# Kernel optimization log

Measured on AMD Instinct MI355X. Metric: run time of the kernel, lower is better.

The kernel has to match this reference:

```python
import jax, jax.numpy as jnp
import numpy as np

TEMP = 0.5  # temperature from init_kwargs
EPS = 1e-8  # torch.nn.CosineSimilarity eps


def setup_inputs() -> dict:
    key = jax.random.key(0)
    k1, k2 = jax.random.split(key)
    B, D = 4096, 128
    return {
        "z_i": jax.random.normal(k1, (B, D), dtype=jnp.float32),
        "z_j": jax.random.normal(k2, (B, D), dtype=jnp.float32),
    }


def reference(z_i, z_j):
    B = z_i.shape[0]          # batch_size * world_size
    N = 2 * B
    z = jnp.concatenate([z_i, z_j], axis=0)              # [N, D]
    zn = z / jnp.maximum(jnp.linalg.norm(z, axis=1, keepdims=True), EPS)
    sim = (zn @ zn.T) / TEMP                             # [N, N] cosine sim / temp
    # positives: sim[i, i+B] and sim[i+B, i]
    pos = jnp.concatenate([jnp.diagonal(sim, offset=B), jnp.diagonal(sim, offset=-B)])  # [N]
    # CE with label 0 over [pos, negatives]; since the positive-pair entry equals pos,
    # denominator = sum_{j != i} exp(sim[i, j])  (only the diagonal is excluded)
    eye = jnp.eye(N, dtype=bool)
    sim_masked = jnp.where(eye, -jnp.inf, sim)
    lse = jax.nn.logsumexp(sim_masked, axis=1)           # [N]
    loss = jnp.sum(lse - pos) / N                        # reduction='sum' then /= N
    return loss
```

## Files before the change

kernel.cpp:

```cpp
#include <hip/hip_runtime.h>
#include <hip/hip_bf16.h>


typedef short bfrag __attribute__((ext_vector_type(8)));
typedef float f32x4 __attribute__((ext_vector_type(4)));

static __device__ __forceinline__ unsigned short f2bf_rne(float x) {
    unsigned u = __float_as_uint(x);
    return (unsigned short)((u + 0x7fffu + ((u >> 16) & 1u)) >> 16);
}
static __device__ __forceinline__ float bf2f(unsigned short b) {
    return __uint_as_float(((unsigned)b) << 16);
}

__global__ __launch_bounds__(256) void nt_norm_pair(
        const float* __restrict__ zi, const float* __restrict__ zj,
        unsigned short* __restrict__ zn, float* __restrict__ diag,
        float* __restrict__ pos, float* __restrict__ sumexp) {
    constexpr int B = 4096, D = 128;
    const int wave = threadIdx.x >> 6, lane = threadIdx.x & 63;
    const int p = blockIdx.x * 4 + wave;
    float2 a = reinterpret_cast<const float2*>(zi + (size_t)p * D)[lane];
    float2 b = reinterpret_cast<const float2*>(zj + (size_t)p * D)[lane];
    float sa = a.x * a.x + a.y * a.y;
    float sb = b.x * b.x + b.y * b.y;
    #pragma unroll
    for (int m = 32; m; m >>= 1) { sa += __shfl_xor(sa, m); sb += __shfl_xor(sb, m); }
    float ia = 1.f / fmaxf(sqrtf(sa), 1e-8f);
    float ib = 1.f / fmaxf(sqrtf(sb), 1e-8f);
    unsigned short a0 = f2bf_rne(a.x * ia), a1 = f2bf_rne(a.y * ia);
    unsigned short b0 = f2bf_rne(b.x * ib), b1 = f2bf_rne(b.y * ib);
    float fa0 = bf2f(a0), fa1 = bf2f(a1), fb0 = bf2f(b0), fb1 = bf2f(b1);
    float da = fa0 * fa0 + fa1 * fa1;
    float db = fb0 * fb0 + fb1 * fb1;
    float cr = fa0 * fb0 + fa1 * fb1;
    #pragma unroll
    for (int m = 32; m; m >>= 1) {
        da += __shfl_xor(da, m); db += __shfl_xor(db, m); cr += __shfl_xor(cr, m);
    }
    reinterpret_cast<unsigned*>(zn + (size_t)p * D)[lane] =
        (unsigned)a0 | ((unsigned)a1 << 16);
    reinterpret_cast<unsigned*>(zn + (size_t)(p + B) * D)[lane] =
        (unsigned)b0 | ((unsigned)b1 << 16);
    if (lane == 0) {
        diag[p] = da; diag[p + B] = db;
        pos[p] = 2.f * cr; pos[p + B] = 2.f * cr;
        sumexp[p] = 0.f; sumexp[p + B] = 0.f;
    }
}

__global__ __launch_bounds__(256, 2) void nt_gram_sym(
        const unsigned short* __restrict__ zn, float* __restrict__ sumexp) {
    const int c = blockIdx.x;
    const int y = blockIdx.y;
    const int T  = (y == 0) ? 1 : ((y == 8 && c >= 32) ? 3 : 4);
    const int d0 = (y == 0) ? 0 : 4 * (y - 1) + 1;

    __shared__ short buf[2][128][128];

    const short* zs = (const short*)zn;
    const int tid = threadIdx.x, wid = tid >> 6, lane = tid & 63;
    const int wj = wid >> 1, wi = wid & 1;
    const int lr = lane & 15, lk = lane >> 4;

    bfrag ca[4][4];
    {
        const int rbase = c * 128 + wj * 64;
        #pragma unroll
        for (int ks = 0; ks < 4; ++ks)
            #pragma unroll
            for (int f = 0; f < 4; ++f)
                ca[ks][f] = *reinterpret_cast<const bfrag*>(
                    zs + (size_t)(rbase + f * 16 + lr) * 128 + ks * 32 + lk * 8);
    }
    asm volatile("s_waitcnt vmcnt(0)" ::: "memory");

    auto STAGE = [&](int t, int slot) {
        const int srow = ((c + d0 + t) & 63) * 128;
        #pragma unroll
        for (int q = 0; q < 8; ++q) {
            const int cbase = (q * 4 + wid) * 64;
            const int chunk = cbase + lane;
            const int r = chunk >> 4;
            const int cpos = chunk & 15;
            const int csrc = cpos ^ (r & 7);
            const short* g = zs + (size_t)(srow + r) * 128 + csrc * 8;
            __builtin_amdgcn_global_load_lds(
                (const __attribute__((address_space(1))) void*)g,
                (__attribute__((address_space(3))) void*)(
                    &buf[slot][0][0] + (size_t)cbase * 8),
                16, 0, 0);
        }
    };

    STAGE(0, 0);

    constexpr float K_E = 2.8853900817779268f;
    float jp[16];
    #pragma unroll
    for (int q = 0; q < 16; ++q) jp[q] = 0.f;

    for (int t = 0; t < T; ++t) {
        const bool more = (t + 1 < T);
        if (more) STAGE(t + 1, (t + 1) & 1);
        if (t == 0) {
            if (more) asm volatile("s_waitcnt vmcnt(8)" ::: "memory");
            else      asm volatile("s_waitcnt vmcnt(0)" ::: "memory");
        } else {
            if (more) asm volatile("s_waitcnt vmcnt(12)" ::: "memory");
            else      asm volatile("s_waitcnt vmcnt(4)" ::: "memory");
        }
        __builtin_amdgcn_s_barrier();

        const int srow = ((c + d0 + t) & 63) * 128;
        f32x4 acc[4][4] = {};
        #pragma unroll
        for (int ks = 0; ks < 4; ++ks) {
            bfrag cb[4];
            #pragma unroll
            for (int f = 0; f < 4; ++f) {
                const int r = wi * 64 + f * 16 + lr;
                const int cc = (ks * 4 + lk) ^ (lr & 7);
                cb[f] = *reinterpret_cast<const bfrag*>(&buf[t & 1][r][cc * 8]);
            }
            #pragma unroll
            for (int fj = 0; fj < 4; ++fj)
                #pragma unroll
                for (int fi = 0; fi < 4; ++fi)
                    acc[fj][fi] = __builtin_amdgcn_mfma_f32_16x16x32_bf16(
                        ca[ks][fj], cb[fi], acc[fj][fi], 0, 0, 0);
        }

        const float cw = (d0 + t) ? 1.f : 0.f;
        #pragma unroll
        for (int fi = 0; fi < 4; ++fi) {
            float s = 0.f;
            #pragma unroll
            for (int fj = 0; fj < 4; ++fj)
                #pragma unroll
                for (int r = 0; r < 4; ++r) {
                    const float e = exp2f(acc[fj][fi][r] * K_E);
                    s += e;
                    jp[fj * 4 + r] += e * cw;
                }
            s += __shfl_xor(s, 16);
            s += __shfl_xor(s, 32);
            if (lk == 0) atomicAdd(&sumexp[srow + wi * 64 + fi * 16 + lr], s);
        }
        __builtin_amdgcn_s_barrier();
    }

    float myv = 0.f;
    #pragma unroll
    for (int tt = 0; tt < 16; ++tt) {
        float v = jp[tt];
        v += __shfl_xor(v, 1);
        v += __shfl_xor(v, 2);
        v += __shfl_xor(v, 4);
        v += __shfl_xor(v, 8);
        if (lr == tt) myv = v;
    }
    atomicAdd(&sumexp[c * 128 + wj * 64 + (lr >> 2) * 16 + lk * 4 + (lr & 3)], myv);
}

__global__ __launch_bounds__(1024) void nt_finalize(
        const float* __restrict__ sumexp, const float* __restrict__ diag,
        const float* __restrict__ pos, float* __restrict__ out) {
    constexpr int N = 8192;
    constexpr float K_E = 2.8853900817779268f;
    float s = 0.f;
    for (int i = threadIdx.x; i < N; i += 1024)
        s += __logf(sumexp[i] - exp2f(diag[i] * K_E)) - pos[i];
    #pragma unroll
    for (int m = 32; m; m >>= 1) s += __shfl_xor(s, m);
    __shared__ float red[16];
    if ((threadIdx.x & 63) == 0) red[threadIdx.x >> 6] = s;
    __syncthreads();
    if (threadIdx.x == 0) {
        float t = 0.f;
        #pragma unroll
        for (int w = 0; w < 16; ++w) t += red[w];
        out[0] = t * (1.0f / (float)N);
    }
}

extern "C" void kernel_launch(void* const* d_in, const int* in_sizes, int n_in,
                              void* d_out, int out_size, void* d_ws, size_t ws_size,
                              hipStream_t stream) {
    const float* zi = (const float*)d_in[0];
    const float* zj = (const float*)d_in[1];
    float* out = (float*)d_out;

    char* ws = (char*)d_ws;
    unsigned short* zn = (unsigned short*)ws;
    float* sumexp = (float*)(ws + 2 * 1024 * 1024);
    float* diag   = (float*)(ws + 2 * 1024 * 1024 + 1 * 32768);
    float* pos    = (float*)(ws + 2 * 1024 * 1024 + 2 * 32768);

    nt_norm_pair<<<1024, 256, 0, stream>>>(zi, zj, zn, diag, pos, sumexp);
    nt_gram_sym<<<dim3(64, 9), 256, 0, stream>>>(zn, sumexp);
    nt_finalize<<<1, 1024, 0, stream>>>(sumexp, diag, pos, out);
}
```

Before: 37.88 us.

## Shrink gram tiles to 64 rows, prescale operand by exp2 constant

```diff
diff --git a/kernel.cpp b/kernel.cpp
--- a/kernel.cpp
+++ b/kernel.cpp
@@ -15,9 +15,11 @@
 
 __global__ __launch_bounds__(256) void nt_norm_pair(
         const float* __restrict__ zi, const float* __restrict__ zj,
-        unsigned short* __restrict__ zn, float* __restrict__ diag,
-        float* __restrict__ pos, float* __restrict__ sumexp) {
+        unsigned short* __restrict__ zn, unsigned short* __restrict__ znK,
+        float* __restrict__ diag, float* __restrict__ pos,
+        float* __restrict__ sumexp) {
     constexpr int B = 4096, D = 128;
+    constexpr float K_E = 2.8853900817779268f;
     const int wave = threadIdx.x >> 6, lane = threadIdx.x & 63;
     const int p = blockIdx.x * 4 + wave;
     float2 a = reinterpret_cast<const float2*>(zi + (size_t)p * D)[lane];
@@ -31,17 +33,23 @@
     unsigned short a0 = f2bf_rne(a.x * ia), a1 = f2bf_rne(a.y * ia);
     unsigned short b0 = f2bf_rne(b.x * ib), b1 = f2bf_rne(b.y * ib);
     float fa0 = bf2f(a0), fa1 = bf2f(a1), fb0 = bf2f(b0), fb1 = bf2f(b1);
-    float da = fa0 * fa0 + fa1 * fa1;
-    float db = fb0 * fb0 + fb1 * fb1;
+    unsigned short aK0 = f2bf_rne(K_E * fa0), aK1 = f2bf_rne(K_E * fa1);
+    unsigned short bK0 = f2bf_rne(K_E * fb0), bK1 = f2bf_rne(K_E * fb1);
+    float da = bf2f(aK0) * fa0 + bf2f(aK1) * fa1;
+    float db = bf2f(bK0) * fb0 + bf2f(bK1) * fb1;
     float cr = fa0 * fb0 + fa1 * fb1;
     #pragma unroll
     for (int m = 32; m; m >>= 1) {
         da += __shfl_xor(da, m); db += __shfl_xor(db, m); cr += __shfl_xor(cr, m);
     }
-    reinterpret_cast<unsigned*>(zn + (size_t)p * D)[lane] =
+    reinterpret_cast<unsigned*>(zn  + (size_t)p * D)[lane] =
         (unsigned)a0 | ((unsigned)a1 << 16);
-    reinterpret_cast<unsigned*>(zn + (size_t)(p + B) * D)[lane] =
+    reinterpret_cast<unsigned*>(zn  + (size_t)(p + B) * D)[lane] =
         (unsigned)b0 | ((unsigned)b1 << 16);
+    reinterpret_cast<unsigned*>(znK + (size_t)p * D)[lane] =
+        (unsigned)aK0 | ((unsigned)aK1 << 16);
+    reinterpret_cast<unsigned*>(znK + (size_t)(p + B) * D)[lane] =
+        (unsigned)bK0 | ((unsigned)bK1 << 16);
     if (lane == 0) {
         diag[p] = da; diag[p + B] = db;
         pos[p] = 2.f * cr; pos[p + B] = 2.f * cr;
@@ -49,37 +57,39 @@
     }
 }
 
-__global__ __launch_bounds__(256, 2) void nt_gram_sym(
-        const unsigned short* __restrict__ zn, float* __restrict__ sumexp) {
+__global__ __launch_bounds__(256, 4) void nt_gram_sym(
+        const unsigned short* __restrict__ zn,
+        const unsigned short* __restrict__ znK,
+        float* __restrict__ sumexp) {
     const int c = blockIdx.x;
     const int y = blockIdx.y;
-    const int T  = (y == 0) ? 1 : ((y == 8 && c >= 32) ? 3 : 4);
+    const int T  = (y == 0) ? 1 : ((y == 16 && c >= 64) ? 3 : 4);
     const int d0 = (y == 0) ? 0 : 4 * (y - 1) + 1;
 
-    __shared__ short buf[2][128][128];
-
-    const short* zs = (const short*)zn;
+    __shared__ short buf[2][64][128];
+
+    const short* zs  = (const short*)zn;
+    const short* zsK = (const short*)znK;
     const int tid = threadIdx.x, wid = tid >> 6, lane = tid & 63;
-    const int wj = wid >> 1, wi = wid & 1;
     const int lr = lane & 15, lk = lane >> 4;
 
     bfrag ca[4][4];
     {
-        const int rbase = c * 128 + wj * 64;
+        const int rbase = c * 64;
         #pragma unroll
         for (int ks = 0; ks < 4; ++ks)
             #pragma unroll
-            for (int f = 0; f < 4; ++f)
-                ca[ks][f] = *reinterpret_cast<const bfrag*>(
-                    zs + (size_t)(rbase + f * 16 + lr) * 128 + ks * 32 + lk * 8);
+            for (int fj = 0; fj < 4; ++fj)
+                ca[ks][fj] = *reinterpret_cast<const bfrag*>(
+                    zsK + (size_t)(rbase + fj * 16 + lr) * 128 + ks * 32 + lk * 8);
     }
     asm volatile("s_waitcnt vmcnt(0)" ::: "memory");
 
     auto STAGE = [&](int t, int slot) {
-        const int srow = ((c + d0 + t) & 63) * 128;
-        #pragma unroll
-        for (int q = 0; q < 8; ++q) {
-            const int cbase = (q * 4 + wid) * 64;
+        const int srow = ((c + d0 + t) & 127) * 64;
+        #pragma unroll
+        for (int q = 0; q < 4; ++q) {
+            const int cbase = q * 256 + wid * 64;
             const int chunk = cbase + lane;
             const int r = chunk >> 4;
             const int cpos = chunk & 15;
@@ -95,7 +105,6 @@
 
     STAGE(0, 0);
 
-    constexpr float K_E = 2.8853900817779268f;
     float jp[16];
     #pragma unroll
     for (int q = 0; q < 16; ++q) jp[q] = 0.f;
@@ -104,73 +113,64 @@
         const bool more = (t + 1 < T);
         if (more) STAGE(t + 1, (t + 1) & 1);
         if (t == 0) {
-            if (more) asm volatile("s_waitcnt vmcnt(8)" ::: "memory");
+            if (more) asm volatile("s_waitcnt vmcnt(4)" ::: "memory");
             else      asm volatile("s_waitcnt vmcnt(0)" ::: "memory");
         } else {
-            if (more) asm volatile("s_waitcnt vmcnt(12)" ::: "memory");
-            else      asm volatile("s_waitcnt vmcnt(4)" ::: "memory");
+            if (more) asm volatile("s_waitcnt vmcnt(5)" ::: "memory");
+            else      asm volatile("s_waitcnt vmcnt(1)" ::: "memory");
         }
         __builtin_amdgcn_s_barrier();
 
-        const int srow = ((c + d0 + t) & 63) * 128;
-        f32x4 acc[4][4] = {};
+        const int srow = ((c + d0 + t) & 127) * 64;
+        f32x4 acc[4] = {};
         #pragma unroll
         for (int ks = 0; ks < 4; ++ks) {
-            bfrag cb[4];
-            #pragma unroll
-            for (int f = 0; f < 4; ++f) {
-                const int r = wi * 64 + f * 16 + lr;
-                const int cc = (ks * 4 + lk) ^ (lr & 7);
-                cb[f] = *reinterpret_cast<const bfrag*>(&buf[t & 1][r][cc * 8]);
-            }
+            const int r = wid * 16 + lr;
+            const int cc = (ks * 4 + lk) ^ (lr & 7);
+            bfrag cb = *reinterpret_cast<const bfrag*>(&buf[t & 1][r][cc * 8]);
             #pragma unroll
             for (int fj = 0; fj < 4; ++fj)
-                #pragma unroll
-                for (int fi = 0; fi < 4; ++fi)
-                    acc[fj][fi] = __builtin_amdgcn_mfma_f32_16x16x32_bf16(
-                        ca[ks][fj], cb[fi], acc[fj][fi], 0, 0, 0);
-        }
-
-        const float cw = (d0 + t) ? 1.f : 0.f;
-        #pragma unroll
-        for (int fi = 0; fi < 4; ++fi) {
-            float s = 0.f;
+                acc[fj] = __builtin_amdgcn_mfma_f32_16x16x32_bf16(
+                    ca[ks][fj], cb, acc[fj], 0, 0, 0);
+        }
+
+        float s = 0.f;
+        #pragma unroll
+        for (int fj = 0; fj < 4; ++fj)
             #pragma unroll
-            for (int fj = 0; fj < 4; ++fj)
-                #pragma unroll
-                for (int r = 0; r < 4; ++r) {
-                    const float e = exp2f(acc[fj][fi][r] * K_E);
-                    s += e;
-                    jp[fj * 4 + r] += e * cw;
-                }
-            s += __shfl_xor(s, 16);
-            s += __shfl_xor(s, 32);
-            if (lk == 0) atomicAdd(&sumexp[srow + wi * 64 + fi * 16 + lr], s);
-        }
+            for (int r = 0; r < 4; ++r) {
+                const float e = exp2f(acc[fj][r]);
+                s += e;
+                jp[fj * 4 + r] += e;
+            }
+        s += __shfl_xor(s, 16);
+        s += __shfl_xor(s, 32);
+        if (lk == 0) atomicAdd(&sumexp[srow + wid * 16 + lr], s);
         __builtin_amdgcn_s_barrier();
     }
 
-    float myv = 0.f;
-    #pragma unroll
-    for (int tt = 0; tt < 16; ++tt) {
-        float v = jp[tt];
-        v += __shfl_xor(v, 1);
-        v += __shfl_xor(v, 2);
-        v += __shfl_xor(v, 4);
-        v += __shfl_xor(v, 8);
-        if (lr == tt) myv = v;
-    }
-    atomicAdd(&sumexp[c * 128 + wj * 64 + (lr >> 2) * 16 + lk * 4 + (lr & 3)], myv);
+    if (y != 0) {
+        float myv = 0.f;
+        #pragma unroll
+        for (int tt = 0; tt < 16; ++tt) {
+            float v = jp[tt];
+            v += __shfl_xor(v, 1);
+            v += __shfl_xor(v, 2);
+            v += __shfl_xor(v, 4);
+            v += __shfl_xor(v, 8);
+            if (lr == tt) myv = v;
+        }
+        atomicAdd(&sumexp[c * 64 + (lr >> 2) * 16 + lk * 4 + (lr & 3)], myv);
+    }
 }
 
 __global__ __launch_bounds__(1024) void nt_finalize(
         const float* __restrict__ sumexp, const float* __restrict__ diag,
         const float* __restrict__ pos, float* __restrict__ out) {
     constexpr int N = 8192;
-    constexpr float K_E = 2.8853900817779268f;
     float s = 0.f;
     for (int i = threadIdx.x; i < N; i += 1024)
-        s += __logf(sumexp[i] - exp2f(diag[i] * K_E)) - pos[i];
+        s += __logf(sumexp[i] - exp2f(diag[i])) - pos[i];
     #pragma unroll
     for (int m = 32; m; m >>= 1) s += __shfl_xor(s, m);
     __shared__ float red[16];
@@ -192,12 +192,13 @@
     float* out = (float*)d_out;
 
     char* ws = (char*)d_ws;
-    unsigned short* zn = (unsigned short*)ws;
-    float* sumexp = (float*)(ws + 2 * 1024 * 1024);
-    float* diag   = (float*)(ws + 2 * 1024 * 1024 + 1 * 32768);
-    float* pos    = (float*)(ws + 2 * 1024 * 1024 + 2 * 32768);
-
-    nt_norm_pair<<<1024, 256, 0, stream>>>(zi, zj, zn, diag, pos, sumexp);
-    nt_gram_sym<<<dim3(64, 9), 256, 0, stream>>>(zn, sumexp);
+    unsigned short* zn  = (unsigned short*)ws;
+    unsigned short* znK = (unsigned short*)(ws + 2 * 1024 * 1024);
+    float* sumexp = (float*)(ws + 4 * 1024 * 1024);
+    float* diag   = (float*)(ws + 4 * 1024 * 1024 + 1 * 32768);
+    float* pos    = (float*)(ws + 4 * 1024 * 1024 + 2 * 32768);
+
+    nt_norm_pair<<<1024, 256, 0, stream>>>(zi, zj, zn, znK, diag, pos, sumexp);
+    nt_gram_sym<<<dim3(128, 17), 256, 0, stream>>>(zn, znK, sumexp);
     nt_finalize<<<1, 1024, 0, stream>>>(sumexp, diag, pos, out);
 }
```

Measured after the change: 52.50 us. +38.6%, slower.
